# Kernel tuning notes

Measured on AMD Instinct MI355X. Metric: run time of the kernel, lower is better.

The kernel has to match this reference:

```python
import jax, jax.numpy as jnp
import numpy as np

B, S, H = 1, 2048, 1024
NH, NKV, HD = 16, 4, 64
I, E, K = 2816, 8, 2
WIN = 512
EPS = 1e-5


def setup_inputs() -> dict:
    key = jax.random.key(0)
    ks = jax.random.split(key, 8)
    sd = 0.02
    return {
        "hidden_states": jax.random.normal(ks[0], (B, S, H), jnp.float32),
        "positions": jnp.arange(S, dtype=jnp.int64),
        "w_qkv": jax.random.normal(ks[1], ((NH + 2 * NKV) * HD, H), jnp.float32) * sd,
        "w_o": jax.random.normal(ks[2], (H, NH * HD), jnp.float32) * sd,
        "router_w": jax.random.normal(ks[3], (E, H), jnp.float32) * sd,
        "ws": jax.random.normal(ks[4], (E, 2 * I, H), jnp.float32) * sd,
        "w2s": jax.random.normal(ks[5], (E, H, I), jnp.float32) * sd,
        "ln1_w": jnp.ones((H,), jnp.float32),
        "ln2_w": jnp.ones((H,), jnp.float32),
    }


def _rmsnorm(x, w):
    return x * jax.lax.rsqrt(jnp.mean(x * x, axis=-1, keepdims=True) + EPS) * w


def reference(hidden_states, positions, w_qkv, w_o, router_w, ws, w2s, ln1_w, ln2_w):
    # residual is None on entry -> residual = input, then input_layernorm
    residual = hidden_states
    x = _rmsnorm(hidden_states, ln1_w)

    # qkv projection (torch Linear: y = x @ W.T), GQA split
    qkv = jnp.einsum("bsh,oh->bso", x, w_qkv)
    q_size, kv_size = NH * HD, NKV * HD
    q = qkv[..., :q_size].reshape(B, S, NH, HD)
    k = qkv[..., q_size:q_size + kv_size].reshape(B, S, NKV, HD)
    v = qkv[..., q_size + kv_size:].reshape(B, S, NKV, HD)
    rep = NH // NKV
    k = jnp.repeat(k, rep, axis=2)  # [B,S,NH,HD]
    v = jnp.repeat(v, rep, axis=2)

    scale = HD ** -0.5
    scores = jnp.einsum("bqhd,bkhd->bhqk", q, k) * scale
    i = jnp.arange(S)[:, None]
    j = jnp.arange(S)[None, :]
    mask = (j <= i) & ((i - j) < WIN)  # causal sliding window
    scores = jnp.where(mask, scores, jnp.finfo(scores.dtype).min)
    attn = jax.nn.softmax(scores, axis=-1)
    o = jnp.einsum("bhqk,bkhd->bqhd", attn, v).reshape(B, S, NH * HD)
    attn_out = jnp.einsum("bso,ho->bsh", o, w_o)

    # pre_moe_layernorm with residual: x += residual; residual = x; x = norm(x)
    x2 = attn_out + residual
    residual2 = x2
    h = _rmsnorm(x2, ln2_w)

    # MoE: router softmax, top-k (renormalize=False), per-expert SwiGLU FFN
    t = h.reshape(-1, H)  # [T,H]
    logits = jnp.einsum("th,eh->te", t, router_w)
    probs = jax.nn.softmax(logits, axis=-1)
    vals, idx = jax.lax.top_k(probs, K)  # [T,K]
    w_dense = jnp.sum(vals[:, :, None] * jax.nn.one_hot(idx, E, dtype=t.dtype), axis=1)  # [T,E]

    out = jnp.zeros_like(t)
    for e in range(E):
        gu = jnp.einsum("th,ih->ti", t, ws[e])  # [T,2I]
        g, u = gu[:, :I], gu[:, I:]
        a = jax.nn.silu(g) * u
        y = jnp.einsum("ti,hi->th", a, w2s[e])
        out = out + w_dense[:, e:e + 1] * y

    return out.reshape(B, S, H), residual2
```

## Files before the change

kernel.cpp:

```cpp
#include <hip/hip_runtime.h>
#include <stdint.h>

typedef unsigned short u16;
typedef __attribute__((ext_vector_type(8))) short short8;
typedef __attribute__((ext_vector_type(4))) float f32x4;

constexpr int SEQ   = 2048;
constexpr int HID   = 1024;
constexpr int NHEAD = 16;
constexpr int QKVD  = 1536;
constexpr int FFI   = 2816;
constexpr int NEXP  = 8;
constexpr int WINSZ = 512;
#define EPSF 1e-5f

__device__ __forceinline__ u16 f2bf(float f) {
  union { unsigned int i; float f; } v; v.f = f;
  unsigned int i = v.i;
  return (u16)((i + 0x7fffu + ((i >> 16) & 1u)) >> 16);
}

__device__ __forceinline__ void gload_lds16(const void* g, void* l) {
  __builtin_amdgcn_global_load_lds((__attribute__((address_space(1))) void*)g,
                                   (__attribute__((address_space(3))) void*)l,
                                   16, 0, 0);
}

#define MFMA_BF16(a, b, c) __builtin_amdgcn_mfma_f32_16x16x32_bf16(a, b, c, 0, 0, 0)

#define PIPE_WAIT(N)                                        \
  asm volatile("s_waitcnt vmcnt(" #N ")" ::: "memory");     \
  __builtin_amdgcn_s_barrier();                             \
  __builtin_amdgcn_sched_barrier(0);
#define PIPE_END                                            \
  __builtin_amdgcn_sched_barrier(0);                        \
  __builtin_amdgcn_s_barrier();

constexpr int CN1 = QKVD * HID / 4;
constexpr int CN2 = HID * HID / 4;
constexpr int CN3 = NEXP * 2 * FFI * HID / 4;
constexpr int CN4 = NEXP * HID * FFI / 4;
constexpr int CN_SMALL = CN1 + CN2;
constexpr int CN_BIG   = CN3 + CN4;
constexpr int NCONV_BLK = CN_BIG / 1024;
constexpr int NATTN_BLK = (SEQ / 64) * NHEAD;

__global__ __launch_bounds__(256) void k_prep(
    const float* __restrict__ x, const float* __restrict__ w, u16* __restrict__ y,
    const float* __restrict__ wqkv, const float* __restrict__ wo,
    u16* __restrict__ dq, u16* __restrict__ dwo) {
  const int bid = blockIdx.x, tid = threadIdx.x;
  __shared__ float red[4];
  if (bid < SEQ) {
    const int wid = tid >> 6, lane = tid & 63;
    const float* xr = x + (size_t)bid * HID;
    float4 v = *(const float4*)&xr[tid * 4];
    float ss = v.x * v.x + v.y * v.y + v.z * v.z + v.w * v.w;
#pragma unroll
    for (int m = 1; m < 64; m <<= 1) ss += __shfl_xor(ss, m);
    if (lane == 0) red[wid] = ss;
    __syncthreads();
    ss = red[0] + red[1] + red[2] + red[3];
    float sc = rsqrtf(ss * (1.0f / HID) + EPSF);
    float4 wv = *(const float4*)&w[tid * 4];
    ushort4 o;
    o.x = f2bf(v.x * sc * wv.x);
    o.y = f2bf(v.y * sc * wv.y);
    o.z = f2bf(v.z * sc * wv.z);
    o.w = f2bf(v.w * sc * wv.w);
    *(ushort4*)&y[(size_t)bid * HID + tid * 4] = o;
    return;
  }
  int j = (bid - SEQ) * 1024 + tid;
#pragma unroll
  for (int t = 0; t < 4; ++t) {
    int i = j + t * 256;
    const float* s; u16* d;
    if (i < CN1) { s = wqkv; d = dq; } else { i -= CN1; s = wo; d = dwo; }
    float4 v = ((const float4*)s)[i];
    ushort4 o;
    o.x = f2bf(v.x); o.y = f2bf(v.y); o.z = f2bf(v.z); o.w = f2bf(v.w);
    ((ushort4*)d)[i] = o;
  }
}

__global__ __launch_bounds__(256, 2) void k_gemm_bt(
    const u16* __restrict__ A, const u16* __restrict__ B,
    void* __restrict__ Cout, int N, int K, int KT, int wf32) {
  __shared__ u16 As[2][128 * 64];
  __shared__ u16 Bs[2][64 * 64];
  const int tid = threadIdx.x, wid = tid >> 6, lane = tid & 63;
  const int quad = lane >> 4, l16 = lane & 15;
  const int wr = wid >> 1, wc = wid & 1;
  const int m0 = blockIdx.y * 128, n0 = blockIdx.x * 64;
  const int M = gridDim.y * 128;
  const int kbase = blockIdx.z * KT * 64;
  const int sr = lane >> 3, sc = (lane & 7) * 8;
  f32x4 acc[4][2] = {};

#define GSTAGE(buf, k0)                                                             \
  {                                                                                 \
    _Pragma("unroll") for (int it = 0; it < 4; ++it) {                              \
      int seg = wid * 4 + it;                                                       \
      int row = seg * 8 + sr;                                                       \
      gload_lds16(&A[(size_t)(m0 + row) * K + (k0) + sc], &As[buf][seg * 512]);     \
    }                                                                               \
    _Pragma("unroll") for (int it = 0; it < 2; ++it) {                              \
      int seg = wid * 2 + it;                                                       \
      int row = seg * 8 + sr;                                                       \
      gload_lds16(&B[(size_t)(n0 + row) * K + (k0) + sc], &Bs[buf][seg * 512]);     \
    }                                                                               \
  }
#define GCOMP(buf)                                                                  \
  {                                                                                 \
    _Pragma("unroll") for (int ks = 0; ks < 2; ++ks) {                              \
      short8 af[4], bf[2];                                                          \
      _Pragma("unroll") for (int t = 0; t < 4; ++t)                                 \
        af[t] = *(const short8*)&As[buf][(64 * wr + 16 * t + l16) * 64 + ks * 32 +  \
                                         quad * 8];                                 \
      _Pragma("unroll") for (int t = 0; t < 2; ++t)                                 \
        bf[t] = *(const short8*)&Bs[buf][(32 * wc + 16 * t + l16) * 64 + ks * 32 +  \
                                         quad * 8];                                 \
      _Pragma("unroll") for (int mt = 0; mt < 4; ++mt)                              \
        _Pragma("unroll") for (int nt = 0; nt < 2; ++nt)                            \
            acc[mt][nt] = MFMA_BF16(af[mt], bf[nt], acc[mt][nt]);                   \
    }                                                                               \
  }

  GSTAGE(0, kbase);
  int cur = 0;
  for (int kt = 0; kt < KT - 1; ++kt) {
    GSTAGE(cur ^ 1, kbase + ((kt + 1) << 6));
    PIPE_WAIT(6)
    GCOMP(cur);
    PIPE_END
    cur ^= 1;
  }
  PIPE_WAIT(0)
  GCOMP(cur);
#undef GSTAGE
#undef GCOMP
  if (wf32) {
    float* C = (float*)Cout + (size_t)blockIdx.z * M * N;
#pragma unroll
    for (int mt = 0; mt < 4; ++mt)
#pragma unroll
      for (int r = 0; r < 4; ++r) {
        int row = m0 + 64 * wr + 16 * mt + quad * 4 + r;
#pragma unroll
        for (int nt = 0; nt < 2; ++nt) {
          int col = n0 + 32 * wc + 16 * nt + l16;
          C[(size_t)row * N + col] = acc[mt][nt][r];
        }
      }
  } else {
    u16* C = (u16*)Cout;
#pragma unroll
    for (int mt = 0; mt < 4; ++mt)
#pragma unroll
      for (int r = 0; r < 4; ++r) {
        int row = m0 + 64 * wr + 16 * mt + quad * 4 + r;
#pragma unroll
        for (int nt = 0; nt < 2; ++nt) {
          int col = n0 + 32 * wc + 16 * nt + l16;
          C[(size_t)row * N + col] = f2bf(acc[mt][nt][r]);
        }
      }
  }
}

__global__ __launch_bounds__(256, 2) void k_attn_conv(
    const u16* __restrict__ qkv, u16* __restrict__ o,
    const float* __restrict__ ws, const float* __restrict__ w2s,
    u16* __restrict__ dws, u16* __restrict__ dw2) {
  const int bid = blockIdx.x;
  const int tid = threadIdx.x;
  if (bid >= NATTN_BLK) {
    int j = (bid - NATTN_BLK) * 1024 + tid;
#pragma unroll
    for (int t = 0; t < 4; ++t) {
      int i = j + t * 256;
      const float* s; u16* d;
      if (i < CN3) { s = ws; d = dws; } else { i -= CN3; s = w2s; d = dw2; }
      float4 v = ((const float4*)s)[i];
      ushort4 u;
      u.x = f2bf(v.x); u.y = f2bf(v.y); u.z = f2bf(v.z); u.w = f2bf(v.w);
      ((ushort4*)d)[i] = u;
    }
    return;
  }
  const int qb = bid & 31;
  const int h  = bid >> 5;
  const int q0 = qb * 64;
  const int g = h >> 2;
  __shared__ u16 Qs[64 * 72], Ks[64 * 72], Vt[64 * 72], Ps[64 * 72];
  const int wid = tid >> 6, lane = tid & 63;
  const int quad = lane >> 4, l16 = lane & 15;

#pragma unroll
  for (int it = 0; it < 2; ++it) {
    int idx = it * 256 + tid;
    int row = idx >> 3, c8 = (idx & 7) * 8;
    *(short8*)&Qs[row * 72 + c8] =
        *(const short8*)&qkv[(size_t)(q0 + row) * QKVD + h * 64 + c8];
  }

  f32x4 oacc[4] = {};
  float mrun[4], lrun[4];
#pragma unroll
  for (int r = 0; r < 4; ++r) { mrun[r] = -1e30f; lrun[r] = 0.f; }

  const int ktlo = (q0 >= WINSZ) ? ((q0 - WINSZ + 1) >> 6) : 0;
  const int kthi = qb;
  for (int kt = ktlo; kt <= kthi; ++kt) {
#pragma unroll
    for (int it = 0; it < 2; ++it) {
      int idx = it * 256 + tid;
      int row = idx >> 3, c8 = (idx & 7) * 8;
      *(short8*)&Ks[row * 72 + c8] =
          *(const short8*)&qkv[(size_t)(kt * 64 + row) * QKVD + 1024 + g * 64 + c8];
    }
#pragma unroll
    for (int it = 0; it < 8; ++it) {
      int idx = it * 256 + tid;
      int key = idx >> 5;
      int d = (idx & 31) * 2;
      unsigned int u = *(const unsigned int*)&qkv[(size_t)(kt * 64 + key) * QKVD + 1280 + g * 64 + d];
      Vt[d * 72 + key] = (u16)(u & 0xffffu);
      Vt[(d + 1) * 72 + key] = (u16)(u >> 16);
    }
    __syncthreads();

    f32x4 sa[4] = {};
#pragma unroll
    for (int ks = 0; ks < 2; ++ks) {
      short8 af = *(const short8*)&Qs[(16 * wid + l16) * 72 + ks * 32 + quad * 8];
#pragma unroll
      for (int ct = 0; ct < 4; ++ct) {
        short8 bf = *(const short8*)&Ks[(16 * ct + l16) * 72 + ks * 32 + quad * 8];
        sa[ct] = MFMA_BF16(af, bf, sa[ct]);
      }
    }

    float pvv[4][4];
#pragma unroll
    for (int r = 0; r < 4; ++r) {
      int i = q0 + 16 * wid + quad * 4 + r;
      float mx = -1e30f;
#pragma unroll
      for (int ct = 0; ct < 4; ++ct) {
        int j = kt * 64 + 16 * ct + l16;
        float v = sa[ct][r] * 0.125f;
        bool ok = (j <= i) && (i - j < WINSZ);
        v = ok ? v : -1e30f;
        pvv[ct][r] = v;
        mx = fmaxf(mx, v);
      }
#pragma unroll
      for (int m = 1; m < 16; m <<= 1) mx = fmaxf(mx, __shfl_xor(mx, m));
      float mnew = fmaxf(mrun[r], mx);
      float alpha = __expf(mrun[r] - mnew);
      float s = 0.f;
#pragma unroll
      for (int ct = 0; ct < 4; ++ct) {
        float p = (pvv[ct][r] > -1e29f) ? __expf(pvv[ct][r] - mnew) : 0.f;
        pvv[ct][r] = p;
        s += p;
      }
#pragma unroll
      for (int m = 1; m < 16; m <<= 1) s += __shfl_xor(s, m);
      lrun[r] = lrun[r] * alpha + s;
      mrun[r] = mnew;
#pragma unroll
      for (int ct = 0; ct < 4; ++ct) oacc[ct][r] *= alpha;
    }
#pragma unroll
    for (int ct = 0; ct < 4; ++ct)
#pragma unroll
      for (int r = 0; r < 4; ++r)
        Ps[(16 * wid + quad * 4 + r) * 72 + 16 * ct + l16] = f2bf(pvv[ct][r]);
    __syncthreads();

#pragma unroll
    for (int ks = 0; ks < 2; ++ks) {
      short8 af = *(const short8*)&Ps[(16 * wid + l16) * 72 + ks * 32 + quad * 8];
#pragma unroll
      for (int ct = 0; ct < 4; ++ct) {
        short8 bf = *(const short8*)&Vt[(16 * ct + l16) * 72 + ks * 32 + quad * 8];
        oacc[ct] = MFMA_BF16(af, bf, oacc[ct]);
      }
    }
    __syncthreads();
  }

#pragma unroll
  for (int ct = 0; ct < 4; ++ct)
#pragma unroll
    for (int r = 0; r < 4; ++r) {
      int row = q0 + 16 * wid + quad * 4 + r;
      float v = oacc[ct][r] / lrun[r];
      o[(size_t)row * HID + h * 64 + 16 * ct + l16] = f2bf(v);
    }
}

__global__ __launch_bounds__(256) void k_rms2_router(
    const float* __restrict__ o0, const float* __restrict__ o1,
    const float* __restrict__ hs, const float* __restrict__ ln2,
    const float* __restrict__ rw, float* __restrict__ out1,
    u16* __restrict__ T, int* __restrict__ counts,
    int* __restrict__ tok_idx, int* __restrict__ tok_slot,
    float* __restrict__ tok_pw) {
  const int tkn = blockIdx.x, tid = threadIdx.x, wid = tid >> 6, lane = tid & 63;
  const size_t base = (size_t)tkn * HID + tid * 4;
  float4 a = *(const float4*)&o0[base];
  float4 b = *(const float4*)&o1[base];
  float4 h = *(const float4*)&hs[base];
  float4 v;
  v.x = a.x + b.x + h.x; v.y = a.y + b.y + h.y;
  v.z = a.z + b.z + h.z; v.w = a.w + b.w + h.w;
  *(float4*)&out1[base] = v;
  float ss = v.x * v.x + v.y * v.y + v.z * v.z + v.w * v.w;
#pragma unroll
  for (int m = 1; m < 64; m <<= 1) ss += __shfl_xor(ss, m);
  __shared__ float red[4];
  if (lane == 0) red[wid] = ss;
  __syncthreads();
  ss = red[0] + red[1] + red[2] + red[3];
  float sc = rsqrtf(ss * (1.0f / HID) + EPSF);
  float4 lw = *(const float4*)&ln2[tid * 4];
  float t0 = v.x * sc * lw.x;
  float t1 = v.y * sc * lw.y;
  float t2 = v.z * sc * lw.z;
  float t3 = v.w * sc * lw.w;
  ushort4 o;
  o.x = f2bf(t0); o.y = f2bf(t1); o.z = f2bf(t2); o.w = f2bf(t3);
  *(ushort4*)&T[(size_t)tkn * HID + tid * 4] = o;

  float p[8];
#pragma unroll
  for (int e = 0; e < 8; ++e) {
    float4 r = *(const float4*)&rw[e * HID + tid * 4];
    p[e] = t0 * r.x + t1 * r.y + t2 * r.z + t3 * r.w;
  }
#pragma unroll
  for (int e = 0; e < 8; ++e)
#pragma unroll
    for (int m = 1; m < 64; m <<= 1) p[e] += __shfl_xor(p[e], m);
  __shared__ float pr[4][8];
  if (lane == 0)
#pragma unroll
    for (int e = 0; e < 8; ++e) pr[wid][e] = p[e];
  __syncthreads();
  if (tid == 0) {
    float lg[8];
#pragma unroll
    for (int e = 0; e < 8; ++e) lg[e] = pr[0][e] + pr[1][e] + pr[2][e] + pr[3][e];
    float mx = lg[0];
#pragma unroll
    for (int e = 1; e < 8; ++e) mx = fmaxf(mx, lg[e]);
    float ex[8], se = 0.f;
#pragma unroll
    for (int e = 0; e < 8; ++e) { ex[e] = __expf(lg[e] - mx); se += ex[e]; }
    int b0 = 0;
#pragma unroll
    for (int e = 1; e < 8; ++e) if (lg[e] > lg[b0]) b0 = e;
    int b1 = (b0 == 0) ? 1 : 0;
#pragma unroll
    for (int e = 0; e < 8; ++e) if (e != b0 && lg[e] > lg[b1]) b1 = e;
    float inv = 1.0f / se;
    int s0 = atomicAdd(&counts[b0], 1);
    tok_idx[b0 * SEQ + s0] = tkn;
    tok_slot[2 * tkn] = b0 * SEQ + s0;
    tok_pw[2 * tkn] = ex[b0] * inv;
    int s1 = atomicAdd(&counts[b1], 1);
    tok_idx[b1 * SEQ + s1] = tkn;
    tok_slot[2 * tkn + 1] = b1 * SEQ + s1;
    tok_pw[2 * tkn + 1] = ex[b1] * inv;
  }
}

__global__ void k_offsets(const int* __restrict__ counts, int* __restrict__ offs) {
  if (threadIdx.x == 0 && blockIdx.x == 0) {
    int s = 0;
    for (int e = 0; e < NEXP; ++e) { offs[e] = s; s += counts[e]; }
    offs[NEXP] = s;
  }
}

__global__ __launch_bounds__(512, 2) void k_moe_gu(
    const u16* __restrict__ T, const u16* __restrict__ Wgu,
    const int* __restrict__ counts, const int* __restrict__ offs,
    const int* __restrict__ tok_idx, u16* __restrict__ Abuf) {
  const int e = blockIdx.z;
  const int cnt = counts[e];
  const int m0 = blockIdx.y * 256;
  if (m0 >= cnt) return;
  const int n0 = blockIdx.x * 64;
  const u16* We = Wgu + (size_t)e * 2 * FFI * HID;
  const int* ti = tok_idx + e * SEQ;
  const int aoff = offs[e];
  __shared__ u16 As[2][256 * 64], Bg[2][64 * 64], Bu[2][64 * 64];
  const int tid = threadIdx.x, wid = tid >> 6, lane = tid & 63;
  const int quad = lane >> 4, l16 = lane & 15;
  const int wr = wid >> 1, wc = wid & 1;
  const int sr = lane >> 3, sc = (lane & 7) * 8;
  int tokrow[4];
#pragma unroll
  for (int it = 0; it < 4; ++it) {
    int row = (wid * 4 + it) * 8 + sr;
    int ra = m0 + row;
    if (ra > cnt - 1) ra = cnt - 1;
    tokrow[it] = ti[ra];
  }
  f32x4 accg[4][2] = {}, accu[4][2] = {};

#define MSTAGE(buf, k0)                                                              \
  {                                                                                  \
    _Pragma("unroll") for (int it = 0; it < 4; ++it) {                               \
      int seg = wid * 4 + it;                                                        \
      gload_lds16(&T[(size_t)tokrow[it] * HID + (k0) + sc], &As[buf][seg * 512]);    \
    }                                                                                \
    {                                                                                \
      int row = wid * 8 + sr;                                                        \
      gload_lds16(&We[(size_t)(n0 + row) * HID + (k0) + sc], &Bg[buf][wid * 512]);   \
      gload_lds16(&We[(size_t)(FFI + n0 + row) * HID + (k0) + sc],                   \
                  &Bu[buf][wid * 512]);                                              \
    }                                                                                \
  }
#define MCOMP(buf)                                                                   \
  {                                                                                  \
    _Pragma("unroll") for (int ks = 0; ks < 2; ++ks) {                               \
      short8 af[4], bg[2], bu[2];                                                    \
      _Pragma("unroll") for (int t = 0; t < 4; ++t)                                  \
        af[t] = *(const short8*)&As[buf][(64 * wr + 16 * t + l16) * 64 + ks * 32 +   \
                                         quad * 8];                                  \
      _Pragma("unroll") for (int t = 0; t < 2; ++t) {                                \
        bg[t] = *(const short8*)&Bg[buf][(32 * wc + 16 * t + l16) * 64 + ks * 32 +   \
                                         quad * 8];                                  \
        bu[t] = *(const short8*)&Bu[buf][(32 * wc + 16 * t + l16) * 64 + ks * 32 +   \
                                         quad * 8];                                  \
      }                                                                              \
      _Pragma("unroll") for (int mt = 0; mt < 4; ++mt)                               \
        _Pragma("unroll") for (int nt = 0; nt < 2; ++nt) {                           \
          accg[mt][nt] = MFMA_BF16(af[mt], bg[nt], accg[mt][nt]);                    \
          accu[mt][nt] = MFMA_BF16(af[mt], bu[nt], accu[mt][nt]);                    \
        }                                                                            \
    }                                                                                \
  }

  MSTAGE(0, 0);
  int cur = 0;
  for (int kt = 0; kt < 15; ++kt) {
    MSTAGE(cur ^ 1, (kt + 1) << 6);
    PIPE_WAIT(6)
    MCOMP(cur);
    PIPE_END
    cur ^= 1;
  }
  PIPE_WAIT(0)
  MCOMP(cur);
#undef MSTAGE
#undef MCOMP
#pragma unroll
  for (int mt = 0; mt < 4; ++mt)
#pragma unroll
    for (int r = 0; r < 4; ++r) {
      int rl = 64 * wr + 16 * mt + quad * 4 + r;
      int grow = m0 + rl;
      if (grow < cnt) {
        size_t rbase = (size_t)(aoff + grow) * FFI;
#pragma unroll
        for (int nt = 0; nt < 2; ++nt) {
          int col = n0 + 32 * wc + 16 * nt + l16;
          float gv = accg[mt][nt][r];
          float uv = accu[mt][nt][r];
          float a = gv / (1.0f + __expf(-gv)) * uv;
          Abuf[rbase + col] = f2bf(a);
        }
      }
    }
}

__global__ __launch_bounds__(256, 2) void k_moe_y(
    const u16* __restrict__ Abuf, const u16* __restrict__ W2,
    const int* __restrict__ counts, const int* __restrict__ offs,
    float* __restrict__ ybuf) {
  const int e = blockIdx.z >> 1;
  const int sk = blockIdx.z & 1;
  const int cnt = counts[e];
  const int m0 = blockIdx.y * 128;
  if (m0 >= cnt) return;
  const int n0 = blockIdx.x * 128;
  const int kbase = sk * 1408;
  const u16* We = W2 + (size_t)e * HID * FFI;
  const int aoff = offs[e];
  __shared__ u16 As[2][128 * 64], Bs[2][128 * 64];
  const int tid = threadIdx.x, wid = tid >> 6, lane = tid & 63;
  const int quad = lane >> 4, l16 = lane & 15;
  const int wr = wid >> 1, wc = wid & 1;
  const int sr = lane >> 3, sc = (lane & 7) * 8;
  int arow[4];
#pragma unroll
  for (int it = 0; it < 4; ++it) {
    int row = (wid * 4 + it) * 8 + sr;
    int ra = m0 + row;
    if (ra > cnt - 1) ra = cnt - 1;
    arow[it] = aoff + ra;
  }
  f32x4 acc[4][4] = {};

#define YSTAGE(buf, k0)                                                              \
  {                                                                                  \
    _Pragma("unroll") for (int it = 0; it < 4; ++it) {                               \
      int seg = wid * 4 + it;                                                        \
      int row = seg * 8 + sr;                                                        \
      gload_lds16(&Abuf[(size_t)arow[it] * FFI + (k0) + sc], &As[buf][seg * 512]);   \
      gload_lds16(&We[(size_t)(n0 + row) * FFI + (k0) + sc], &Bs[buf][seg * 512]);   \
    }                                                                                \
  }
#define YCOMP(buf)                                                                   \
  {                                                                                  \
    _Pragma("unroll") for (int ks = 0; ks < 2; ++ks) {                               \
      short8 af[4], bf[4];                                                           \
      _Pragma("unroll") for (int t = 0; t < 4; ++t)                                  \
        af[t] = *(const short8*)&As[buf][(64 * wr + 16 * t + l16) * 64 + ks * 32 +   \
                                         quad * 8];                                  \
      _Pragma("unroll") for (int t = 0; t < 4; ++t)                                  \
        bf[t] = *(const short8*)&Bs[buf][(64 * wc + 16 * t + l16) * 64 + ks * 32 +   \
                                         quad * 8];                                  \
      _Pragma("unroll") for (int mt = 0; mt < 4; ++mt)                               \
        _Pragma("unroll") for (int nt = 0; nt < 4; ++nt)                             \
            acc[mt][nt] = MFMA_BF16(af[mt], bf[nt], acc[mt][nt]);                    \
    }                                                                                \
  }

  YSTAGE(0, kbase);
  int cur = 0;
  for (int kt = 0; kt < 21; ++kt) {
    YSTAGE(cur ^ 1, kbase + ((kt + 1) << 6));
    PIPE_WAIT(8)
    YCOMP(cur);
    PIPE_END
    cur ^= 1;
  }
  PIPE_WAIT(0)
  YCOMP(cur);
#undef YSTAGE
#undef YCOMP
  float* Y = ybuf + (size_t)sk * 2 * SEQ * HID;
#pragma unroll
  for (int mt = 0; mt < 4; ++mt)
#pragma unroll
    for (int r = 0; r < 4; ++r) {
      int rl = 64 * wr + 16 * mt + quad * 4 + r;
      int grow = m0 + rl;
      if (grow < cnt) {
        size_t obase = (size_t)(aoff + grow) * HID;
#pragma unroll
        for (int nt = 0; nt < 4; ++nt) {
          int col = n0 + 64 * wc + 16 * nt + l16;
          Y[obase + col] = acc[mt][nt][r];
        }
      }
    }
}

__global__ __launch_bounds__(256) void k_moe_out(
    const float* __restrict__ yb, const int* __restrict__ offs,
    const int* __restrict__ tok_slot, const float* __restrict__ tok_pw,
    float* __restrict__ out0) {
  const int t = blockIdx.x, tid = threadIdx.x;
  const int v0 = tok_slot[2 * t], v1 = tok_slot[2 * t + 1];
  const float w0 = tok_pw[2 * t], w1 = tok_pw[2 * t + 1];
  const size_t g0 = (size_t)(offs[v0 >> 11] + (v0 & (SEQ - 1))) * HID;
  const size_t g1 = (size_t)(offs[v1 >> 11] + (v1 & (SEQ - 1))) * HID;
  const size_t YP = (size_t)2 * SEQ * HID;
  const int c = tid * 4;
  float4 a0 = *(const float4*)&yb[g0 + c];
  float4 b0 = *(const float4*)&yb[YP + g0 + c];
  float4 a1 = *(const float4*)&yb[g1 + c];
  float4 b1 = *(const float4*)&yb[YP + g1 + c];
  float4 r;
  r.x = w0 * (a0.x + b0.x) + w1 * (a1.x + b1.x);
  r.y = w0 * (a0.y + b0.y) + w1 * (a1.y + b1.y);
  r.z = w0 * (a0.z + b0.z) + w1 * (a1.z + b1.z);
  r.w = w0 * (a0.w + b0.w) + w1 * (a1.w + b1.w);
  *(float4*)&out0[(size_t)t * HID + c] = r;
}

extern "C" void kernel_launch(void* const* d_in, const int* in_sizes, int n_in,
                              void* d_out, int out_size, void* d_ws, size_t ws_size,
                              hipStream_t stream) {
  const float* hs   = (const float*)d_in[0];
  const float* wqkv = (const float*)d_in[2];
  const float* wo   = (const float*)d_in[3];
  const float* rwt  = (const float*)d_in[4];
  const float* wsx  = (const float*)d_in[5];
  const float* w2s  = (const float*)d_in[6];
  const float* ln1  = (const float*)d_in[7];
  const float* ln2  = (const float*)d_in[8];
  float* out0 = (float*)d_out;
  float* out1 = out0 + (size_t)SEQ * HID;

  char* p = (char*)d_ws;
  u16* xn       = (u16*)p;   p += (size_t)SEQ * HID * 2;
  u16* qkv      = (u16*)p;   p += (size_t)SEQ * QKVD * 2;
  u16* ob       = (u16*)p;   p += (size_t)SEQ * HID * 2;
  float* of     = (float*)p; p += (size_t)2 * SEQ * HID * 4;
  int* counts   = (int*)p;   p += 32;
  int* offs     = (int*)p;   p += 64;
  int* tok_idx  = (int*)p;   p += (size_t)NEXP * SEQ * 4;
  int* tok_slot = (int*)p;   p += (size_t)2 * SEQ * 4;
  float* tok_pw = (float*)p; p += (size_t)2 * SEQ * 4;
  u16* abuf     = (u16*)p;   p += (size_t)2 * SEQ * FFI * 2;
  float* ybuf   = (float*)p; p += (size_t)2 * 2 * SEQ * HID * 4;
  u16* wqkv_b   = (u16*)p;   p += (size_t)QKVD * HID * 2;
  u16* wo_b     = (u16*)p;   p += (size_t)HID * HID * 2;
  u16* ws_b     = (u16*)p;   p += (size_t)NEXP * 2 * FFI * HID * 2;
  u16* w2s_b    = (u16*)p;   p += (size_t)NEXP * HID * FFI * 2;

  u16* tb = xn;

  hipMemsetAsync(counts, 0, 32, stream);

  k_prep<<<SEQ + CN_SMALL / 1024, 256, 0, stream>>>(
      hs, ln1, xn, wqkv, wo, wqkv_b, wo_b);
  k_gemm_bt<<<dim3(QKVD / 64, SEQ / 128, 1), 256, 0, stream>>>(
      xn, wqkv_b, qkv, QKVD, HID, 16, 0);
  k_attn_conv<<<NATTN_BLK + NCONV_BLK, 256, 0, stream>>>(
      qkv, ob, wsx, w2s, ws_b, w2s_b);
  k_gemm_bt<<<dim3(HID / 64, SEQ / 128, 2), 256, 0, stream>>>(
      ob, wo_b, of, HID, HID, 8, 1);
  k_rms2_router<<<SEQ, 256, 0, stream>>>(of, of + (size_t)SEQ * HID, hs, ln2,
                                         rwt, out1, tb, counts, tok_idx,
                                         tok_slot, tok_pw);
  k_offsets<<<1, 64, 0, stream>>>(counts, offs);
  k_moe_gu<<<dim3(FFI / 64, SEQ / 256, NEXP), 512, 0, stream>>>(
      tb, ws_b, counts, offs, tok_idx, abuf);
  k_moe_y<<<dim3(HID / 128, SEQ / 128, NEXP * 2), 256, 0, stream>>>(
      abuf, w2s_b, counts, offs, ybuf);
  k_moe_out<<<SEQ, 256, 0, stream>>>(ybuf, offs, tok_slot, tok_pw, out0);
}
```

Measured before the change: 659.2 us.

## Fuse fp32 weight conversion into dense GEMM and enlarge MoE tiles

The dense GEMM now reads fp32 weights directly, converts them to bf16 in registers and stores them in padded LDS, which drops the separate qkv/o weight conversion pass from k_prep. That GEMM loses its double-buffered async pipeline and becomes single-buffered with two syncthreads per k-step. Both MoE kernels double their N tile per block (gate/up to 128, down to 256 with 512 threads) to raise reuse of the A tile. Their prefetch schedule also changes from a partial vmcnt wait to a full drain before each tile, which may reduce overlap of loads with MFMA work.

```diff
diff --git a/kernel.cpp b/kernel.cpp
--- a/kernel.cpp
+++ b/kernel.cpp
@@ -20,6 +20,12 @@
   return (u16)((i + 0x7fffu + ((i >> 16) & 1u)) >> 16);
 }
 
+__device__ __forceinline__ ushort4 f2bf4(float4 v) {
+  ushort4 o;
+  o.x = f2bf(v.x); o.y = f2bf(v.y); o.z = f2bf(v.z); o.w = f2bf(v.w);
+  return o;
+}
+
 __device__ __forceinline__ void gload_lds16(const void* g, void* l) {
   __builtin_amdgcn_global_load_lds((__attribute__((address_space(1))) void*)g,
                                    (__attribute__((address_space(3))) void*)l,
@@ -28,67 +34,46 @@
 
 #define MFMA_BF16(a, b, c) __builtin_amdgcn_mfma_f32_16x16x32_bf16(a, b, c, 0, 0, 0)
 
-#define PIPE_WAIT(N)                                        \
-  asm volatile("s_waitcnt vmcnt(" #N ")" ::: "memory");     \
+#define TILE_FENCE                                          \
+  asm volatile("s_waitcnt vmcnt(0)" ::: "memory");          \
   __builtin_amdgcn_s_barrier();                             \
   __builtin_amdgcn_sched_barrier(0);
-#define PIPE_END                                            \
-  __builtin_amdgcn_sched_barrier(0);                        \
-  __builtin_amdgcn_s_barrier();
-
-constexpr int CN1 = QKVD * HID / 4;
-constexpr int CN2 = HID * HID / 4;
+
 constexpr int CN3 = NEXP * 2 * FFI * HID / 4;
 constexpr int CN4 = NEXP * HID * FFI / 4;
-constexpr int CN_SMALL = CN1 + CN2;
 constexpr int CN_BIG   = CN3 + CN4;
 constexpr int NCONV_BLK = CN_BIG / 1024;
 constexpr int NATTN_BLK = (SEQ / 64) * NHEAD;
 
-__global__ __launch_bounds__(256) void k_prep(
-    const float* __restrict__ x, const float* __restrict__ w, u16* __restrict__ y,
-    const float* __restrict__ wqkv, const float* __restrict__ wo,
-    u16* __restrict__ dq, u16* __restrict__ dwo) {
+__global__ __launch_bounds__(256) void k_prep(const float* __restrict__ x,
+                                              const float* __restrict__ w,
+                                              u16* __restrict__ y) {
   const int bid = blockIdx.x, tid = threadIdx.x;
+  const int wid = tid >> 6, lane = tid & 63;
   __shared__ float red[4];
-  if (bid < SEQ) {
-    const int wid = tid >> 6, lane = tid & 63;
-    const float* xr = x + (size_t)bid * HID;
-    float4 v = *(const float4*)&xr[tid * 4];
-    float ss = v.x * v.x + v.y * v.y + v.z * v.z + v.w * v.w;
-#pragma unroll
-    for (int m = 1; m < 64; m <<= 1) ss += __shfl_xor(ss, m);
-    if (lane == 0) red[wid] = ss;
-    __syncthreads();
-    ss = red[0] + red[1] + red[2] + red[3];
-    float sc = rsqrtf(ss * (1.0f / HID) + EPSF);
-    float4 wv = *(const float4*)&w[tid * 4];
-    ushort4 o;
-    o.x = f2bf(v.x * sc * wv.x);
-    o.y = f2bf(v.y * sc * wv.y);
-    o.z = f2bf(v.z * sc * wv.z);
-    o.w = f2bf(v.w * sc * wv.w);
-    *(ushort4*)&y[(size_t)bid * HID + tid * 4] = o;
-    return;
-  }
-  int j = (bid - SEQ) * 1024 + tid;
-#pragma unroll
-  for (int t = 0; t < 4; ++t) {
-    int i = j + t * 256;
-    const float* s; u16* d;
-    if (i < CN1) { s = wqkv; d = dq; } else { i -= CN1; s = wo; d = dwo; }
-    float4 v = ((const float4*)s)[i];
-    ushort4 o;
-    o.x = f2bf(v.x); o.y = f2bf(v.y); o.z = f2bf(v.z); o.w = f2bf(v.w);
-    ((ushort4*)d)[i] = o;
-  }
+  const float* xr = x + (size_t)bid * HID;
+  float4 v = *(const float4*)&xr[tid * 4];
+  float ss = v.x * v.x + v.y * v.y + v.z * v.z + v.w * v.w;
+#pragma unroll
+  for (int m = 1; m < 64; m <<= 1) ss += __shfl_xor(ss, m);
+  if (lane == 0) red[wid] = ss;
+  __syncthreads();
+  ss = red[0] + red[1] + red[2] + red[3];
+  float sc = rsqrtf(ss * (1.0f / HID) + EPSF);
+  float4 wv = *(const float4*)&w[tid * 4];
+  ushort4 o;
+  o.x = f2bf(v.x * sc * wv.x);
+  o.y = f2bf(v.y * sc * wv.y);
+  o.z = f2bf(v.z * sc * wv.z);
+  o.w = f2bf(v.w * sc * wv.w);
+  *(ushort4*)&y[(size_t)bid * HID + tid * 4] = o;
 }
 
 __global__ __launch_bounds__(256, 2) void k_gemm_bt(
-    const u16* __restrict__ A, const u16* __restrict__ B,
+    const u16* __restrict__ A, const float* __restrict__ B,
     void* __restrict__ Cout, int N, int K, int KT, int wf32) {
-  __shared__ u16 As[2][128 * 64];
-  __shared__ u16 Bs[2][64 * 64];
+  __shared__ u16 As[128 * 64];
+  __shared__ u16 Bs[64 * 72];
   const int tid = threadIdx.x, wid = tid >> 6, lane = tid & 63;
   const int quad = lane >> 4, l16 = lane & 15;
   const int wr = wid >> 1, wc = wid & 1;
@@ -96,50 +81,44 @@
   const int M = gridDim.y * 128;
   const int kbase = blockIdx.z * KT * 64;
   const int sr = lane >> 3, sc = (lane & 7) * 8;
+  const int brow = wid * 16 + (lane >> 2);
+  const int bk = (lane & 3) * 16;
   f32x4 acc[4][2] = {};
-
-#define GSTAGE(buf, k0)                                                             \
-  {                                                                                 \
-    _Pragma("unroll") for (int it = 0; it < 4; ++it) {                              \
-      int seg = wid * 4 + it;                                                       \
-      int row = seg * 8 + sr;                                                       \
-      gload_lds16(&A[(size_t)(m0 + row) * K + (k0) + sc], &As[buf][seg * 512]);     \
-    }                                                                               \
-    _Pragma("unroll") for (int it = 0; it < 2; ++it) {                              \
-      int seg = wid * 2 + it;                                                       \
-      int row = seg * 8 + sr;                                                       \
-      gload_lds16(&B[(size_t)(n0 + row) * K + (k0) + sc], &Bs[buf][seg * 512]);     \
-    }                                                                               \
-  }
-#define GCOMP(buf)                                                                  \
-  {                                                                                 \
-    _Pragma("unroll") for (int ks = 0; ks < 2; ++ks) {                              \
-      short8 af[4], bf[2];                                                          \
-      _Pragma("unroll") for (int t = 0; t < 4; ++t)                                 \
-        af[t] = *(const short8*)&As[buf][(64 * wr + 16 * t + l16) * 64 + ks * 32 +  \
-                                         quad * 8];                                 \
-      _Pragma("unroll") for (int t = 0; t < 2; ++t)                                 \
-        bf[t] = *(const short8*)&Bs[buf][(32 * wc + 16 * t + l16) * 64 + ks * 32 +  \
-                                         quad * 8];                                 \
-      _Pragma("unroll") for (int mt = 0; mt < 4; ++mt)                              \
-        _Pragma("unroll") for (int nt = 0; nt < 2; ++nt)                            \
-            acc[mt][nt] = MFMA_BF16(af[mt], bf[nt], acc[mt][nt]);                   \
-    }                                                                               \
-  }
-
-  GSTAGE(0, kbase);
-  int cur = 0;
-  for (int kt = 0; kt < KT - 1; ++kt) {
-    GSTAGE(cur ^ 1, kbase + ((kt + 1) << 6));
-    PIPE_WAIT(6)
-    GCOMP(cur);
-    PIPE_END
-    cur ^= 1;
-  }
-  PIPE_WAIT(0)
-  GCOMP(cur);
-#undef GSTAGE
-#undef GCOMP
+  for (int kt = 0; kt < KT; ++kt) {
+    const int k0 = kbase + (kt << 6);
+    const float* bp = &B[(size_t)(n0 + brow) * K + k0 + bk];
+    float4 bv0 = *(const float4*)&bp[0];
+    float4 bv1 = *(const float4*)&bp[4];
+    float4 bv2 = *(const float4*)&bp[8];
+    float4 bv3 = *(const float4*)&bp[12];
+#pragma unroll
+    for (int it = 0; it < 4; ++it) {
+      int seg = wid * 4 + it;
+      int row = seg * 8 + sr;
+      gload_lds16(&A[(size_t)(m0 + row) * K + k0 + sc], &As[seg * 512]);
+    }
+    *(ushort4*)&Bs[brow * 72 + bk + 0]  = f2bf4(bv0);
+    *(ushort4*)&Bs[brow * 72 + bk + 4]  = f2bf4(bv1);
+    *(ushort4*)&Bs[brow * 72 + bk + 8]  = f2bf4(bv2);
+    *(ushort4*)&Bs[brow * 72 + bk + 12] = f2bf4(bv3);
+    __syncthreads();
+#pragma unroll
+    for (int ks = 0; ks < 2; ++ks) {
+      short8 af[4], bf[2];
+#pragma unroll
+      for (int t = 0; t < 4; ++t)
+        af[t] = *(const short8*)&As[(64 * wr + 16 * t + l16) * 64 + ks * 32 + quad * 8];
+#pragma unroll
+      for (int t = 0; t < 2; ++t)
+        bf[t] = *(const short8*)&Bs[(32 * wc + 16 * t + l16) * 72 + ks * 32 + quad * 8];
+#pragma unroll
+      for (int mt = 0; mt < 4; ++mt)
+#pragma unroll
+        for (int nt = 0; nt < 2; ++nt)
+          acc[mt][nt] = MFMA_BF16(af[mt], bf[nt], acc[mt][nt]);
+    }
+    __syncthreads();
+  }
   if (wf32) {
     float* C = (float*)Cout + (size_t)blockIdx.z * M * N;
 #pragma unroll
@@ -395,14 +374,14 @@
   const int cnt = counts[e];
   const int m0 = blockIdx.y * 256;
   if (m0 >= cnt) return;
-  const int n0 = blockIdx.x * 64;
+  const int n0 = blockIdx.x * 128;
   const u16* We = Wgu + (size_t)e * 2 * FFI * HID;
   const int* ti = tok_idx + e * SEQ;
   const int aoff = offs[e];
-  __shared__ u16 As[2][256 * 64], Bg[2][64 * 64], Bu[2][64 * 64];
+  __shared__ u16 As[2][256 * 64], Bg[2][128 * 64], Bu[2][128 * 64];
   const int tid = threadIdx.x, wid = tid >> 6, lane = tid & 63;
   const int quad = lane >> 4, l16 = lane & 15;
-  const int wr = wid >> 1, wc = wid & 1;
+  const int wr = wid >> 2, wc = wid & 3;
   const int sr = lane >> 3, sc = (lane & 7) * 8;
   int tokrow[4];
 #pragma unroll
@@ -412,7 +391,7 @@
     if (ra > cnt - 1) ra = cnt - 1;
     tokrow[it] = ti[ra];
   }
-  f32x4 accg[4][2] = {}, accu[4][2] = {};
+  f32x4 accg[8][2] = {}, accu[8][2] = {};
 
 #define MSTAGE(buf, k0)                                                              \
   {                                                                                  \
@@ -420,19 +399,20 @@
       int seg = wid * 4 + it;                                                        \
       gload_lds16(&T[(size_t)tokrow[it] * HID + (k0) + sc], &As[buf][seg * 512]);    \
     }                                                                                \
-    {                                                                                \
-      int row = wid * 8 + sr;                                                        \
-      gload_lds16(&We[(size_t)(n0 + row) * HID + (k0) + sc], &Bg[buf][wid * 512]);   \
+    _Pragma("unroll") for (int it = 0; it < 2; ++it) {                               \
+      int seg = wid * 2 + it;                                                        \
+      int row = seg * 8 + sr;                                                        \
+      gload_lds16(&We[(size_t)(n0 + row) * HID + (k0) + sc], &Bg[buf][seg * 512]);   \
       gload_lds16(&We[(size_t)(FFI + n0 + row) * HID + (k0) + sc],                   \
-                  &Bu[buf][wid * 512]);                                              \
+                  &Bu[buf][seg * 512]);                                              \
     }                                                                                \
   }
 #define MCOMP(buf)                                                                   \
   {                                                                                  \
     _Pragma("unroll") for (int ks = 0; ks < 2; ++ks) {                               \
-      short8 af[4], bg[2], bu[2];                                                    \
-      _Pragma("unroll") for (int t = 0; t < 4; ++t)                                  \
-        af[t] = *(const short8*)&As[buf][(64 * wr + 16 * t + l16) * 64 + ks * 32 +   \
+      short8 af[8], bg[2], bu[2];                                                    \
+      _Pragma("unroll") for (int t = 0; t < 8; ++t)                                  \
+        af[t] = *(const short8*)&As[buf][(128 * wr + 16 * t + l16) * 64 + ks * 32 +  \
                                          quad * 8];                                  \
       _Pragma("unroll") for (int t = 0; t < 2; ++t) {                                \
         bg[t] = *(const short8*)&Bg[buf][(32 * wc + 16 * t + l16) * 64 + ks * 32 +   \
@@ -440,7 +420,7 @@
         bu[t] = *(const short8*)&Bu[buf][(32 * wc + 16 * t + l16) * 64 + ks * 32 +   \
                                          quad * 8];                                  \
       }                                                                              \
-      _Pragma("unroll") for (int mt = 0; mt < 4; ++mt)                               \
+      _Pragma("unroll") for (int mt = 0; mt < 8; ++mt)                               \
         _Pragma("unroll") for (int nt = 0; nt < 2; ++nt) {                           \
           accg[mt][nt] = MFMA_BF16(af[mt], bg[nt], accg[mt][nt]);                    \
           accu[mt][nt] = MFMA_BF16(af[mt], bu[nt], accu[mt][nt]);                    \
@@ -449,23 +429,21 @@
   }
 
   MSTAGE(0, 0);
+  TILE_FENCE
   int cur = 0;
-  for (int kt = 0; kt < 15; ++kt) {
-    MSTAGE(cur ^ 1, (kt + 1) << 6);
-    PIPE_WAIT(6)
+  for (int kt = 0; kt < 16; ++kt) {
+    if (kt + 1 < 16) MSTAGE(cur ^ 1, (kt + 1) << 6);
     MCOMP(cur);
-    PIPE_END
+    if (kt + 1 < 16) { TILE_FENCE }
     cur ^= 1;
   }
-  PIPE_WAIT(0)
-  MCOMP(cur);
 #undef MSTAGE
 #undef MCOMP
 #pragma unroll
-  for (int mt = 0; mt < 4; ++mt)
+  for (int mt = 0; mt < 8; ++mt)
 #pragma unroll
     for (int r = 0; r < 4; ++r) {
-      int rl = 64 * wr + 16 * mt + quad * 4 + r;
+      int rl = 128 * wr + 16 * mt + quad * 4 + r;
       int grow = m0 + rl;
       if (grow < cnt) {
         size_t rbase = (size_t)(aoff + grow) * FFI;
@@ -481,7 +459,7 @@
     }
 }
 
-__global__ __launch_bounds__(256, 2) void k_moe_y(
+__global__ __launch_bounds__(512, 2) void k_moe_y(
     const u16* __restrict__ Abuf, const u16* __restrict__ W2,
     const int* __restrict__ counts, const int* __restrict__ offs,
     float* __restrict__ ybuf) {
@@ -490,19 +468,19 @@
   const int cnt = counts[e];
   const int m0 = blockIdx.y * 128;
   if (m0 >= cnt) return;
-  const int n0 = blockIdx.x * 128;
+  const int n0 = blockIdx.x * 256;
   const int kbase = sk * 1408;
   const u16* We = W2 + (size_t)e * HID * FFI;
   const int aoff = offs[e];
-  __shared__ u16 As[2][128 * 64], Bs[2][128 * 64];
+  __shared__ u16 As[2][128 * 64], Bs[2][256 * 64];
   const int tid = threadIdx.x, wid = tid >> 6, lane = tid & 63;
   const int quad = lane >> 4, l16 = lane & 15;
-  const int wr = wid >> 1, wc = wid & 1;
+  const int wr = wid >> 2, wc = wid & 3;
   const int sr = lane >> 3, sc = (lane & 7) * 8;
-  int arow[4];
-#pragma unroll
-  for (int it = 0; it < 4; ++it) {
-    int row = (wid * 4 + it) * 8 + sr;
+  int arow[2];
+#pragma unroll
+  for (int it = 0; it < 2; ++it) {
+    int row = (wid * 2 + it) * 8 + sr;
     int ra = m0 + row;
     if (ra > cnt - 1) ra = cnt - 1;
     arow[it] = aoff + ra;
@@ -511,10 +489,13 @@
 
 #define YSTAGE(buf, k0)                                                              \
   {                                                                                  \
+    _Pragma("unroll") for (int it = 0; it < 2; ++it) {                               \
+      int seg = wid * 2 + it;                                                        \
+      gload_lds16(&Abuf[(size_t)arow[it] * FFI + (k0) + sc], &As[buf][seg * 512]);   \
+    }                                                                                \
     _Pragma("unroll") for (int it = 0; it < 4; ++it) {                               \
       int seg = wid * 4 + it;                                                        \
       int row = seg * 8 + sr;                                                        \
-      gload_lds16(&Abuf[(size_t)arow[it] * FFI + (k0) + sc], &As[buf][seg * 512]);   \
       gload_lds16(&We[(size_t)(n0 + row) * FFI + (k0) + sc], &Bs[buf][seg * 512]);   \
     }                                                                                \
   }
@@ -535,16 +516,14 @@
   }
 
   YSTAGE(0, kbase);
+  TILE_FENCE
   int cur = 0;
-  for (int kt = 0; kt < 21; ++kt) {
-    YSTAGE(cur ^ 1, kbase + ((kt + 1) << 6));
-    PIPE_WAIT(8)
+  for (int kt = 0; kt < 22; ++kt) {
+    if (kt + 1 < 22) YSTAGE(cur ^ 1, kbase + ((kt + 1) << 6));
     YCOMP(cur);
-    PIPE_END
+    if (kt + 1 < 22) { TILE_FENCE }
     cur ^= 1;
   }
-  PIPE_WAIT(0)
-  YCOMP(cur);
 #undef YSTAGE
 #undef YCOMP
   float* Y = ybuf + (size_t)sk * 2 * SEQ * HID;
@@ -614,8 +593,6 @@
   float* tok_pw = (float*)p; p += (size_t)2 * SEQ * 4;
   u16* abuf     = (u16*)p;   p += (size_t)2 * SEQ * FFI * 2;
   float* ybuf   = (float*)p; p += (size_t)2 * 2 * SEQ * HID * 4;
-  u16* wqkv_b   = (u16*)p;   p += (size_t)QKVD * HID * 2;
-  u16* wo_b     = (u16*)p;   p += (size_t)HID * HID * 2;
   u16* ws_b     = (u16*)p;   p += (size_t)NEXP * 2 * FFI * HID * 2;
   u16* w2s_b    = (u16*)p;   p += (size_t)NEXP * HID * FFI * 2;
 
@@ -623,21 +600,20 @@
 
   hipMemsetAsync(counts, 0, 32, stream);
 
-  k_prep<<<SEQ + CN_SMALL / 1024, 256, 0, stream>>>(
-      hs, ln1, xn, wqkv, wo, wqkv_b, wo_b);
+  k_prep<<<SEQ, 256, 0, stream>>>(hs, ln1, xn);
   k_gemm_bt<<<dim3(QKVD / 64, SEQ / 128, 1), 256, 0, stream>>>(
-      xn, wqkv_b, qkv, QKVD, HID, 16, 0);
+      xn, wqkv, qkv, QKVD, HID, 16, 0);
   k_attn_conv<<<NATTN_BLK + NCONV_BLK, 256, 0, stream>>>(
       qkv, ob, wsx, w2s, ws_b, w2s_b);
   k_gemm_bt<<<dim3(HID / 64, SEQ / 128, 2), 256, 0, stream>>>(
-      ob, wo_b, of, HID, HID, 8, 1);
+      ob, wo, of, HID, HID, 8, 1);
   k_rms2_router<<<SEQ, 256, 0, stream>>>(of, of + (size_t)SEQ * HID, hs, ln2,
                                          rwt, out1, tb, counts, tok_idx,
                                          tok_slot, tok_pw);
   k_offsets<<<1, 64, 0, stream>>>(counts, offs);
-  k_moe_gu<<<dim3(FFI / 64, SEQ / 256, NEXP), 512, 0, stream>>>(
+  k_moe_gu<<<dim3(FFI / 128, SEQ / 256, NEXP), 512, 0, stream>>>(
       tb, ws_b, counts, offs, tok_idx, abuf);
-  k_moe_y<<<dim3(HID / 128, SEQ / 128, NEXP * 2), 256, 0, stream>>>(
+  k_moe_y<<<dim3(HID / 256, SEQ / 128, NEXP * 2), 512, 0, stream>>>(
       abuf, w2s_b, counts, offs, ybuf);
   k_moe_out<<<SEQ, 256, 0, stream>>>(ybuf, offs, tok_slot, tok_pw, out0);
 }
```

Measured after the change: 678.0 us. +2.8%, slower.
